# Kernel optimization log

Measured on AMD Instinct MI355X. Metric: run time of the kernel, lower is better.

Reference implementation:

```python
import jax, jax.numpy as jnp
import numpy as np

NUM_BINS = 32
SIGMA_RATIO = 0.5          # Gaussian Parzen window width relative to bin spacing
SMOOTH_NR = 1e-07
SMOOTH_DR = 1e-07


def setup_inputs() -> dict:
    key = jax.random.key(0)
    k1, k2 = jax.random.split(key)
    shape = (2, 1, 96, 96, 96)
    pred = jax.random.uniform(k1, shape, dtype=jnp.float32)
    target = jax.random.uniform(k2, shape, dtype=jnp.float32)
    return {"pred": pred, "target": target}


def _parzen_weights(img_flat, bin_centers, preterm):
    # img_flat: [B, N]; bin_centers: [nb]
    # Gaussian Parzen window, normalized so each voxel's weights sum to 1 over bins.
    d = img_flat[..., None] - bin_centers          # [B, N, nb]
    w = jnp.exp(-preterm * d * d)                  # [B, N, nb]
    return w / jnp.sum(w, axis=-1, keepdims=True)


def reference(pred, target):
    B = pred.shape[0]
    nb = NUM_BINS
    bin_centers = jnp.linspace(0.0, 1.0, nb, dtype=jnp.float32)  # [nb]
    bin_width = 1.0 / (nb - 1)
    sigma = SIGMA_RATIO * bin_width
    preterm = jnp.float32(1.0 / (2.0 * sigma * sigma))

    p = pred.reshape(B, -1)    # [B, N]
    t = target.reshape(B, -1)  # [B, N]
    N = p.shape[1]

    wa = _parzen_weights(p, bin_centers, preterm)  # [B, N, nb]
    wb = _parzen_weights(t, bin_centers, preterm)  # [B, N, nb]

    # joint histogram [B, nb, nb] and marginals [B, 1, nb]
    pab = jnp.einsum('bni,bnj->bij', wa, wb) / N
    pa = jnp.mean(wa, axis=1, keepdims=True).transpose(0, 2, 1).transpose(0, 2, 1)  # [B,1,nb]
    pa = jnp.mean(wa, axis=1)[:, None, :]  # [B, 1, nb]
    pb = jnp.mean(wb, axis=1)[:, None, :]  # [B, 1, nb]

    # papb = bmm(pa^T, pb): outer product of marginals -> [B, nb, nb]
    papb = jnp.einsum('bki,bkj->bij', pa, pb)

    mi = jnp.sum(pab * jnp.log((pab + SMOOTH_NR) / (papb + SMOOTH_DR) + SMOOTH_DR),
                 axis=(-1, -2))  # [B]
    return -jnp.mean(mi)
```

## Files before the change

kernel.cpp:

```cpp
#include <hip/hip_runtime.h>
#include <hip/hip_bf16.h>

#define NBINS 32
#define CHUNK 128
#define NROWS 34
#define STR 136
#define TILE_HALVES (NROWS * STR)
#define NTHREADS 256
#define NVOX 884736
#define BPB 768
#define NCHUNKS 9
#define NSLOTS 16

typedef __attribute__((ext_vector_type(8))) _Float16 half8;
typedef __attribute__((ext_vector_type(16))) float f32x16;
typedef __attribute__((ext_vector_type(4))) int i32x4;

__device__ __forceinline__ void compute_w(float x, int& kb, _Float16* wq) {
    float tt = x * 31.0f;
    float kf = rintf(tt);
    int ki = (int)kf;
    float u = tt - kf;
    const bool sp = (u > 0.0f);
    kb = ki - 3 + (sp ? 1 : 0);

    float t1 = __expf(4.0f * u);
    float t2 = t1 * t1;
    float t3 = t2 * t1;
    float t4 = t2 * t2;
    float t5 = t3 * t2;
    float ts = sp ? t1 : 1.0f;
    const float c0 = 1.50343918e-8f;
    const float c1 = 3.35462628e-4f;
    const float c2 = 1.35335283e-1f;
    const float c3 = 1.0f;

    float w[6];
    float s = 0.0f;
    {
        float p0 = 1.0f, p1 = t1, p2 = t2, p3 = t3, p4 = t4, p5 = t5;
        float e;
        e = (sp ? c1 : c0) * p0 * ts; e = ((unsigned)(kb + 0) < NBINS) ? e : 0.0f; w[0] = e; s += e;
        e = (sp ? c2 : c1) * p1 * ts; e = ((unsigned)(kb + 1) < NBINS) ? e : 0.0f; w[1] = e; s += e;
        e = (sp ? c3 : c2) * p2 * ts; e = ((unsigned)(kb + 2) < NBINS) ? e : 0.0f; w[2] = e; s += e;
        e = (sp ? c2 : c3) * p3 * ts; e = ((unsigned)(kb + 3) < NBINS) ? e : 0.0f; w[3] = e; s += e;
        e = (sp ? c1 : c2) * p4 * ts; e = ((unsigned)(kb + 4) < NBINS) ? e : 0.0f; w[4] = e; s += e;
        e = (sp ? c0 : c1) * p5 * ts; e = ((unsigned)(kb + 5) < NBINS) ? e : 0.0f; w[5] = e; s += e;
    }
    float rinv = 1.0f / s;
#pragma unroll
    for (int o = 0; o < 6; ++o) wq[o] = (_Float16)(w[o] * rinv);
}

__device__ __forceinline__ void zero6(_Float16* __restrict__ L, int col, int kb) {
#pragma unroll
    for (int o = 0; o < 6; ++o) {
        int r = min(max(kb + o, -1), 32) + 1;
        L[r * STR + col] = (_Float16)0.0f;
    }
}
__device__ __forceinline__ void scatter6(_Float16* __restrict__ L, int col, int kb,
                                         const _Float16* wq) {
#pragma unroll
    for (int o = 0; o < 6; ++o) {
        int r = min(max(kb + o, -1), 32) + 1;
        L[r * STR + col] = wq[o];
    }
}

__global__ __launch_bounds__(NTHREADS, 6)
void mi_hist_kernel(const float* __restrict__ pred, const float* __restrict__ targ,
                    float* __restrict__ hist ) {
    __shared__ __attribute__((aligned(16))) _Float16 smem[2 * TILE_HALVES];
    _Float16* TA = smem;
    _Float16* TB = smem + TILE_HALVES;

    const int tid = threadIdx.x;
    const int bx = blockIdx.x;
    const int batch = blockIdx.y;
    const int col = tid & 127;
    const float* src = (tid >= 128 ? targ : pred) + (size_t)batch * NVOX;
    _Float16* T = smem + (tid >> 7) * TILE_HALVES;

    const int wid = tid >> 6;
    const int lane = tid & 63;
    const int frag = (1 + (lane & 31)) * STR + wid * 32 + 8 * (lane >> 5);

    float xs[NCHUNKS];
#pragma unroll
    for (int c = 0; c < NCHUNKS; ++c)
        xs[c] = src[((size_t)(c * BPB + bx)) * CHUNK + col];

    {
        i32x4 z = {0, 0, 0, 0};
        i32x4* zp = (i32x4*)smem;
#pragma unroll
        for (int i = 0; i < 5; ++i) {
            int idx = i * NTHREADS + tid;
            if (idx < (2 * TILE_HALVES) / 8) zp[idx] = z;
        }
    }

    f32x16 acc;
#pragma unroll
    for (int r = 0; r < 16; ++r) acc[r] = 0.0f;

    int kb_old = 0;

#define DO_MFMA() { \
        _Pragma("unroll") \
        for (int kk = 0; kk < 2; ++kk) { \
            half8 af = *(const half8*)&TA[frag + kk * 16]; \
            half8 bf = *(const half8*)&TB[frag + kk * 16]; \
            acc = __builtin_amdgcn_mfma_f32_32x32x16_f16(af, bf, acc, 0, 0, 0); \
        } }

    {
        _Float16 wq[6]; int kb;
        compute_w(xs[0], kb, wq);
        __syncthreads();
        scatter6(T, col, kb, wq);
        kb_old = kb;
        __syncthreads();
        DO_MFMA();
    }
#pragma unroll
    for (int c = 1; c < NCHUNKS; ++c) {
        _Float16 wq[6]; int kb;
        compute_w(xs[c], kb, wq);
        __syncthreads();
        zero6(T, col, kb_old);
        scatter6(T, col, kb, wq);
        kb_old = kb;
        __syncthreads();
        DO_MFMA();
    }
    __syncthreads();

    float* red = (float*)smem;
    const int colc = lane & 31;
    const int rlo = 4 * (lane >> 5);
#pragma unroll
    for (int r = 0; r < 16; ++r) {
        int rowc = (r & 3) + 8 * (r >> 2) + rlo;
        red[wid * 1024 + rowc * 32 + colc] = acc[r];
    }
    __syncthreads();
    float* H = hist + ((size_t)(bx & (NSLOTS - 1)) * 2 + batch) * 1024;
    for (int idx = tid; idx < 1024; idx += NTHREADS) {
        float s = red[idx] + red[1024 + idx] + red[2048 + idx] + red[3072 + idx];
        atomicAdd(&H[idx], s);
    }
}

__global__ void mi_reduce_kernel(const float* __restrict__ hist, float* __restrict__ out) {
    __shared__ float s_pab[2 * NBINS * NBINS];
    __shared__ double s_pa[2][NBINS];
    __shared__ double s_pb[2][NBINS];
    __shared__ double s_red[1024];
    const int tid = threadIdx.x;
    const double invN = 1.0 / (double)NVOX;

    for (int g = tid; g < 512; g += 1024) {
        float4 s = make_float4(0.f, 0.f, 0.f, 0.f);
        for (int sl = 0; sl < NSLOTS; ++sl) {
            float4 v = ((const float4*)hist)[sl * 512 + g];
            s.x += v.x; s.y += v.y; s.z += v.z; s.w += v.w;
        }
        ((float4*)s_pab)[g] = s;
    }
    __syncthreads();

    if (tid < 64) {
        int b = tid >> 5, i = tid & 31;
        double s = 0.0;
        for (int j = 0; j < NBINS; ++j) s += (double)s_pab[(b * NBINS + i) * NBINS + j];
        s_pa[b][i] = s * invN;
    } else if (tid < 128) {
        int t2 = tid - 64;
        int b = t2 >> 5, j = t2 & 31;
        double s = 0.0;
        for (int i = 0; i < NBINS; ++i) s += (double)s_pab[(b * NBINS + i) * NBINS + j];
        s_pb[b][j] = s * invN;
    }
    __syncthreads();

    double acc = 0.0;
    for (int idx = tid; idx < 2 * NBINS * NBINS; idx += 1024) {
        int b = idx >> 10;
        int cell = idx & 1023;
        int i = cell >> 5, j = cell & 31;
        double pab = (double)s_pab[idx] * invN;
        double papb = s_pa[b][i] * s_pb[b][j];
        acc += pab * log((pab + 1e-7) / (papb + 1e-7) + 1e-7);
    }
    s_red[tid] = acc;
    __syncthreads();
    for (int s2 = 512; s2 > 0; s2 >>= 1) {
        if (tid < s2) s_red[tid] += s_red[tid + s2];
        __syncthreads();
    }
    if (tid == 0) out[0] = (float)(-0.5 * s_red[0]);
}

extern "C" void kernel_launch(void* const* d_in, const int* in_sizes, int n_in,
                              void* d_out, int out_size, void* d_ws, size_t ws_size,
                              hipStream_t stream) {
    const float* pred = (const float*)d_in[0];
    const float* targ = (const float*)d_in[1];
    float* hist = (float*)d_ws;
    float* out = (float*)d_out;

    hipMemsetAsync(hist, 0, NSLOTS * 2 * NBINS * NBINS * sizeof(float), stream);
    dim3 grid(BPB, 2);
    hipLaunchKernelGGL(mi_hist_kernel, grid, dim3(NTHREADS), 0, stream, pred, targ, hist);
    hipLaunchKernelGGL(mi_reduce_kernel, dim3(1), dim3(1024), 0, stream, hist, out);
}
```

Measured before the change: 30.04 us.

## Ping-pong two warp groups so weight scatter overlaps MFMA accumulation

```diff
diff --git a/kernel.cpp b/kernel.cpp
--- a/kernel.cpp
+++ b/kernel.cpp
@@ -6,10 +6,11 @@
 #define NROWS 34
 #define STR 136
 #define TILE_HALVES (NROWS * STR)
-#define NTHREADS 256
+#define BUF_HALVES (2 * TILE_HALVES)
+#define NTHREADS 512
 #define NVOX 884736
-#define BPB 768
-#define NCHUNKS 9
+#define BPB 384
+#define NCH 9
 #define NSLOTS 16
 
 typedef __attribute__((ext_vector_type(8))) _Float16 half8;
@@ -38,14 +39,13 @@
     float w[6];
     float s = 0.0f;
     {
-        float p0 = 1.0f, p1 = t1, p2 = t2, p3 = t3, p4 = t4, p5 = t5;
         float e;
-        e = (sp ? c1 : c0) * p0 * ts; e = ((unsigned)(kb + 0) < NBINS) ? e : 0.0f; w[0] = e; s += e;
-        e = (sp ? c2 : c1) * p1 * ts; e = ((unsigned)(kb + 1) < NBINS) ? e : 0.0f; w[1] = e; s += e;
-        e = (sp ? c3 : c2) * p2 * ts; e = ((unsigned)(kb + 2) < NBINS) ? e : 0.0f; w[2] = e; s += e;
-        e = (sp ? c2 : c3) * p3 * ts; e = ((unsigned)(kb + 3) < NBINS) ? e : 0.0f; w[3] = e; s += e;
-        e = (sp ? c1 : c2) * p4 * ts; e = ((unsigned)(kb + 4) < NBINS) ? e : 0.0f; w[4] = e; s += e;
-        e = (sp ? c0 : c1) * p5 * ts; e = ((unsigned)(kb + 5) < NBINS) ? e : 0.0f; w[5] = e; s += e;
+        e = (sp ? c1 : c0) * 1.0f * ts; e = ((unsigned)(kb + 0) < NBINS) ? e : 0.0f; w[0] = e; s += e;
+        e = (sp ? c2 : c1) * t1 * ts;   e = ((unsigned)(kb + 1) < NBINS) ? e : 0.0f; w[1] = e; s += e;
+        e = (sp ? c3 : c2) * t2 * ts;   e = ((unsigned)(kb + 2) < NBINS) ? e : 0.0f; w[2] = e; s += e;
+        e = (sp ? c2 : c3) * t3 * ts;   e = ((unsigned)(kb + 3) < NBINS) ? e : 0.0f; w[3] = e; s += e;
+        e = (sp ? c1 : c2) * t4 * ts;   e = ((unsigned)(kb + 4) < NBINS) ? e : 0.0f; w[4] = e; s += e;
+        e = (sp ? c0 : c1) * t5 * ts;   e = ((unsigned)(kb + 5) < NBINS) ? e : 0.0f; w[5] = e; s += e;
     }
     float rinv = 1.0f / s;
 #pragma unroll
@@ -71,25 +71,27 @@
 __global__ __launch_bounds__(NTHREADS, 6)
 void mi_hist_kernel(const float* __restrict__ pred, const float* __restrict__ targ,
                     float* __restrict__ hist ) {
-    __shared__ __attribute__((aligned(16))) _Float16 smem[2 * TILE_HALVES];
-    _Float16* TA = smem;
-    _Float16* TB = smem + TILE_HALVES;
+    __shared__ __attribute__((aligned(16))) _Float16 smem[2 * BUF_HALVES];
 
     const int tid = threadIdx.x;
     const int bx = blockIdx.x;
     const int batch = blockIdx.y;
+    const int g = tid >> 8;
     const int col = tid & 127;
-    const float* src = (tid >= 128 ? targ : pred) + (size_t)batch * NVOX;
-    _Float16* T = smem + (tid >> 7) * TILE_HALVES;
-
-    const int wid = tid >> 6;
+    const int isB = (tid >> 7) & 1;
+    const float* src = (isB ? targ : pred) + (size_t)batch * NVOX;
+    _Float16* T = smem + g * BUF_HALVES + isB * TILE_HALVES;
+    const _Float16* PA = smem + g * BUF_HALVES;
+    const _Float16* PB = PA + TILE_HALVES;
+
     const int lane = tid & 63;
-    const int frag = (1 + (lane & 31)) * STR + wid * 32 + 8 * (lane >> 5);
-
-    float xs[NCHUNKS];
-#pragma unroll
-    for (int c = 0; c < NCHUNKS; ++c)
-        xs[c] = src[((size_t)(c * BPB + bx)) * CHUNK + col];
+    const int gwave = (tid >> 6) & 3;
+    const int frag = (1 + (lane & 31)) * STR + gwave * 32 + 8 * (lane >> 5);
+
+    float xs[NCH];
+#pragma unroll
+    for (int c = 0; c < NCH; ++c)
+        xs[c] = src[((size_t)(c * (2 * BPB) + bx * 2 + g)) * CHUNK + col];
 
     {
         i32x4 z = {0, 0, 0, 0};
@@ -97,7 +99,7 @@
 #pragma unroll
         for (int i = 0; i < 5; ++i) {
             int idx = i * NTHREADS + tid;
-            if (idx < (2 * TILE_HALVES) / 8) zp[idx] = z;
+            if (idx < (2 * BUF_HALVES) / 8) zp[idx] = z;
         }
     }
 
@@ -106,38 +108,46 @@
     for (int r = 0; r < 16; ++r) acc[r] = 0.0f;
 
     int kb_old = 0;
+    const bool isG0 = (g == 0);
 
 #define DO_MFMA() { \
         _Pragma("unroll") \
         for (int kk = 0; kk < 2; ++kk) { \
-            half8 af = *(const half8*)&TA[frag + kk * 16]; \
-            half8 bf = *(const half8*)&TB[frag + kk * 16]; \
+            half8 af = *(const half8*)&PA[frag + kk * 16]; \
+            half8 bf = *(const half8*)&PB[frag + kk * 16]; \
             acc = __builtin_amdgcn_mfma_f32_32x32x16_f16(af, bf, acc, 0, 0, 0); \
         } }
 
-    {
-        _Float16 wq[6]; int kb;
-        compute_w(xs[0], kb, wq);
+#pragma unroll
+    for (int c = 0; c <= NCH; ++c) {
+        _Float16 wq[6]; int kb = 0;
+        if (isG0 && c < NCH) compute_w(xs[c], kb, wq);
         __syncthreads();
-        scatter6(T, col, kb, wq);
-        kb_old = kb;
+        if (isG0) {
+            if (c < NCH) {
+                if (c >= 1) zero6(T, col, kb_old);
+                scatter6(T, col, kb, wq);
+                kb_old = kb;
+            }
+        } else {
+            if (c >= 1) DO_MFMA();
+            if (c < NCH) compute_w(xs[c], kb, wq);
+        }
         __syncthreads();
-        DO_MFMA();
-    }
-#pragma unroll
-    for (int c = 1; c < NCHUNKS; ++c) {
-        _Float16 wq[6]; int kb;
-        compute_w(xs[c], kb, wq);
-        __syncthreads();
-        zero6(T, col, kb_old);
-        scatter6(T, col, kb, wq);
-        kb_old = kb;
-        __syncthreads();
-        DO_MFMA();
-    }
+        if (isG0) {
+            if (c < NCH) DO_MFMA();
+        } else if (c < NCH) {
+            if (c >= 1) zero6(T, col, kb_old);
+            scatter6(T, col, kb, wq);
+            kb_old = kb;
+        }
+    }
+#undef DO_MFMA
+
     __syncthreads();
 
     float* red = (float*)smem;
+    const int wid = tid >> 6;
     const int colc = lane & 31;
     const int rlo = 4 * (lane >> 5);
 #pragma unroll
@@ -148,7 +158,9 @@
     __syncthreads();
     float* H = hist + ((size_t)(bx & (NSLOTS - 1)) * 2 + batch) * 1024;
     for (int idx = tid; idx < 1024; idx += NTHREADS) {
-        float s = red[idx] + red[1024 + idx] + red[2048 + idx] + red[3072 + idx];
+        float s = 0.0f;
+#pragma unroll
+        for (int w = 0; w < 8; ++w) s += red[w * 1024 + idx];
         atomicAdd(&H[idx], s);
     }
 }
```

Result: no change. 30.06 us (+0.1%).
